# Kernel optimization log

Hardware: AMD Instinct MI355X
Metric: run time of the kernel (lower is better)

Reference implementation:

```python
import jax, jax.numpy as jnp
import numpy as np

T, B = 256, 256
OBS, FEAT, A = 512, 512, 15
H = FEAT + A + 1  # lstm_output_size = feature_dim + num_actions + 1 = 528


def setup_inputs() -> dict:
    key = jax.random.key(0)
    ks = jax.random.split(key, 16)
    s = 0.05
    f32 = jnp.float32
    return {
        "obs": jax.random.normal(ks[0], (T, B, OBS), f32),
        "last_action": jax.random.randint(ks[1], (T, B), 0, A, dtype=jnp.int32),
        "reward": jax.random.normal(ks[2], (T, B), f32),
        "terminated": jax.random.bernoulli(ks[3], 0.05, (T, B)),
        # encoder Linear(OBS -> FEAT)
        "W_enc": jax.random.normal(ks[4], (FEAT, OBS), f32) * s,
        "b_enc": jnp.zeros((FEAT,), f32),
        # 2-layer LSTM, input size == hidden size == H, torch gate order i,f,g,o
        "w_ih0": jax.random.normal(ks[5], (4 * H, H), f32) * s,
        "w_hh0": jax.random.normal(ks[6], (4 * H, H), f32) * s,
        "b_ih0": jnp.zeros((4 * H,), f32),
        "b_hh0": jnp.zeros((4 * H,), f32),
        "w_ih1": jax.random.normal(ks[7], (4 * H, H), f32) * s,
        "w_hh1": jax.random.normal(ks[8], (4 * H, H), f32) * s,
        "b_ih1": jnp.zeros((4 * H,), f32),
        "b_hh1": jnp.zeros((4 * H,), f32),
        # heads
        "W_pol": jax.random.normal(ks[9], (A, H), f32) * s,
        "b_pol": jnp.zeros((A,), f32),
        "W_base": jax.random.normal(ks[10], (1, H), f32) * s,
        "b_base": jnp.zeros((1,), f32),
    }


def reference(obs, last_action, reward, terminated,
              W_enc, b_enc,
              w_ih0, w_hh0, b_ih0, b_hh0,
              w_ih1, w_hh1, b_ih1, b_hh1,
              W_pol, b_pol, W_base, b_base):
    Tn, Bn = obs.shape[0], obs.shape[1]
    feats = jax.nn.relu(jnp.einsum('tbo,fo->tbf', obs, W_enc) + b_enc)
    one_hot = jax.nn.one_hot(last_action, A, dtype=feats.dtype)
    clipped_r = jnp.clip(reward, -1.0, 1.0)[..., None]
    x = jnp.concatenate([feats, clipped_r, one_hot], axis=-1)  # [T,B,H]
    nd = (~terminated).astype(x.dtype)[..., None]              # [T,B,1]

    w_ih = (w_ih0, w_ih1)
    w_hh = (w_hh0, w_hh1)
    b_ih = (b_ih0, b_ih1)
    b_hh = (b_hh0, b_hh1)

    def step(carry, inp):
        h, c = carry          # each [2,B,H]
        x_t, nd_t = inp       # [B,H], [B,1]
        h = h * nd_t          # done-mask reset of state, per original loop
        c = c * nd_t
        inp_l = x_t
        new_h, new_c = [], []
        for l in range(2):
            gates = inp_l @ w_ih[l].T + b_ih[l] + h[l] @ w_hh[l].T + b_hh[l]
            i, f, g, o = jnp.split(gates, 4, axis=-1)
            c_l = jax.nn.sigmoid(f) * c[l] + jax.nn.sigmoid(i) * jnp.tanh(g)
            h_l = jax.nn.sigmoid(o) * jnp.tanh(c_l)
            new_h.append(h_l)
            new_c.append(c_l)
            inp_l = h_l
        return (jnp.stack(new_h), jnp.stack(new_c)), inp_l

    h0 = jnp.zeros((2, Bn, H), x.dtype)  # init_state: zeros
    c0 = jnp.zeros((2, Bn, H), x.dtype)
    (hT, cT), lstm_out = jax.lax.scan(step, (h0, c0), (x, nd))  # lstm_out [T,B,H]

    policy_logits = lstm_out @ W_pol.T + b_pol          # [T,B,A]
    baseline = (lstm_out @ W_base.T + b_base)[..., 0]   # [T,B]
    action = jax.random.categorical(jax.random.key(1), policy_logits, axis=-1)  # [T,B]
    return policy_logits, baseline, action, hT, cT
```

## Files before the change

### kernel.cpp

```cpp
#include <hip/hip_runtime.h>
#include <stdint.h>
#include <math.h>

#define TSTEPS 256
#define BATCH  256
#define OBS_D  512
#define FEATD  512
#define NACT   15
#define HDIM   528
#define HB     (HDIM*BATCH)

#define OFF_ND    0
#define OFF_FLAG  65536
#define ALW_BYTES 262208
#define SB        91952
#define FXT       (SB)
#define FH0       (FXT + 4*HB)
#define FH1       (FH0 + 2*HB)
#define FC0       (FH1 + 2*HB)
#define FC1       (FC0 + HB)
#define FST_END   (FC1 + HB)

#define DBS0   0
#define DBS1   2112
#define DBENC  4224
#define DHW    4736
#define DHB    13184
#define DALW_N 13200

#define OUT_POL   0
#define OUT_BASE  983040
#define OUT_ACT   1048576
#define OUT_H     1114112
#define OUT_C     1384448

__device__ __forceinline__ float sigf_(float x){ return 1.0f/(1.0f+expf(-x)); }

__device__ __forceinline__ uint32_t rotl32_(uint32_t x, uint32_t d){
  return (x<<d)|(x>>(32u-d));
}

__device__ double gumbel_for(uint32_t idx){
  uint32_t x0 = 0u, x1 = idx;
  const uint32_t k0 = 0u, k1 = 1u;
  const uint32_t ks[3] = {k0, k1, 0x1BD11BDAu ^ k0 ^ k1};
  x0 += ks[0]; x1 += ks[1];
  const uint32_t R0[4] = {13u,15u,26u,6u}, R1[4] = {17u,29u,16u,24u};
  #pragma unroll
  for (int g=0; g<5; ++g){
    const uint32_t* r = (g&1) ? R1 : R0;
    #pragma unroll
    for (int j=0;j<4;++j){ x0 += x1; x1 = rotl32_(x1, r[j]); x1 ^= x0; }
    x0 += ks[(g+1)%3];
    x1 += ks[(g+2)%3] + (uint32_t)(g+1);
  }
  const uint32_t bits = x0 ^ x1;
  float u = __uint_as_float((bits>>9) | 0x3f800000u) - 1.0f;
  const float TINY = 1.17549435e-38f;
  u = u * (1.0f - TINY) + TINY;
  u = fmaxf(TINY, u);
  return -log(-log((double)u));
}

__global__ void zero_kernel(float* __restrict__ p, int n){
  int i = blockIdx.x*256 + threadIdx.x;
  if (i < n) p[i] = 0.0f;
}

__global__ void detect_term_kernel(const void* __restrict__ term, int* __restrict__ flag){
  __shared__ int s_nf, s_nb, s_ni;
  if (threadIdx.x==0){ s_nf=0; s_nb=0; s_ni=0; }
  __syncthreads();
  const uint8_t*  pb = (const uint8_t*)term;
  const uint32_t* pw = (const uint32_t*)term;
  int nf=0, nb=0, ni=0;
  for (int i=threadIdx.x; i<16384; i+=256){
    uint32_t v = pw[i];
    if (v == 0x3F800000u) nf++;
    if (v == 1u) ni++;
  }
  for (int o=threadIdx.x; o<65536; o+=256){
    if ((o&3) && pb[o]) nb++;
  }
  if (nf) atomicAdd(&s_nf, nf);
  if (nb) atomicAdd(&s_nb, nb);
  if (ni) atomicAdd(&s_ni, ni);
  __syncthreads();
  if (threadIdx.x==0){
    flag[0] = (s_nf>0) ? 2 : ((s_nb>0) ? 0 : ((s_ni>0) ? 1 : 0));
  }
}

__global__ void nd_kernel(const void* __restrict__ term, const int* __restrict__ flag,
                          float* __restrict__ nd){
  int i = blockIdx.x*256 + threadIdx.x;
  if (i >= TSTEPS*BATCH) return;
  int f = flag[0];
  bool done;
  if (f == 0)      done = ((const uint8_t*)term)[i] != 0;
  else if (f == 1) done = ((const int*)term)[i] != 0;
  else             done = ((const float*)term)[i] != 0.0f;
  nd[i] = done ? 0.0f : 1.0f;
}

__global__ void prep_small_kernel(float* __restrict__ alw,
    const float* __restrict__ bih0, const float* __restrict__ bhh0,
    const float* __restrict__ bih1, const float* __restrict__ bhh1,
    const float* __restrict__ benc,
    const float* __restrict__ Wpol, const float* __restrict__ bpol,
    const float* __restrict__ Wbase, const float* __restrict__ bbase){
  int i = blockIdx.x*256 + threadIdx.x;
  if (i >= DALW_N) return;
  if (i < 2112)            alw[DBS0 + i] = bih0[i] + bhh0[i];
  else if (i < 4224)       { int j=i-2112; alw[DBS1 + j] = bih1[j] + bhh1[j]; }
  else if (i < 4736)       { int j=i-4224; alw[DBENC + j] = benc[j]; }
  else if (i < 13184)      { int j=i-4736; int r=j/HDIM, k=j%HDIM;
                             alw[DHW + j] = (r<NACT ? Wpol[r*HDIM+k] : Wbase[k]); }
  else                     { int j=i-13184; alw[DHB + j] = (j<NACT ? bpol[j] : bbase[0]); }
}

__device__ __forceinline__ void lstm_block(
    int jt, int step, const float* __restrict__ srcA, const float* __restrict__ srcB,
    const float* __restrict__ wih, const float* __restrict__ whh,
    const float* __restrict__ bsum,
    const float* __restrict__ nd, float* __restrict__ cbuf, float* __restrict__ hout,
    int b)
{
  const int j0 = jt*2;
  const float ndv = nd[step*BATCH + b];
  float acc[8];
  const float* wA[8]; const float* wB[8];
  #pragma unroll
  for (int c=0;c<8;++c){
    const int col = (c>>1)*HDIM + j0 + (c&1);
    acc[c] = bsum[col];
    wA[c] = wih + (size_t)col*HDIM;
    wB[c] = whh + (size_t)col*HDIM;
  }
  const float* a = srcA + b;
  #pragma unroll 8
  for (int k=0;k<HDIM;++k){
    const float xv = a[(size_t)k*BATCH];
    #pragma unroll
    for (int c=0;c<8;++c) acc[c] = fmaf(wA[c][k], xv, acc[c]);
  }
  const float* bb = srcB + b;
  #pragma unroll 8
  for (int k=0;k<HDIM;++k){
    const float hv = bb[(size_t)k*BATCH] * ndv;
    #pragma unroll
    for (int c=0;c<8;++c) acc[c] = fmaf(wB[c][k], hv, acc[c]);
  }
  #pragma unroll
  for (int jj=0;jj<2;++jj){
    const float gi=acc[0+jj], gf=acc[2+jj], gg=acc[4+jj], go=acc[6+jj];
    const int idx=(j0+jj)*BATCH+b;
    const float cold = cbuf[idx]*ndv;
    const float cn = sigf_(gf)*cold + sigf_(gi)*tanhf(gg);
    const float hn = sigf_(go)*tanhf(cn);
    cbuf[idx]=cn; hout[idx]=hn;
  }
}

__global__ __launch_bounds__(256) void step_kernel(
  const float* __restrict__ obs, const int* __restrict__ lastAct,
  const float* __restrict__ reward,
  const float* __restrict__ wenc,
  const float* __restrict__ wih0, const float* __restrict__ whh0,
  const float* __restrict__ wih1, const float* __restrict__ whh1,
  float* __restrict__ ws, float* __restrict__ alw,
  float* __restrict__ out, int t)
{
  const int bid = blockIdx.x;
  const int b = threadIdx.x;
  float* nd = ws + OFF_ND;
  float* xT = ws + FXT;
  float* h0 = ws + FH0;
  float* h1 = ws + FH1;
  float* c0 = ws + FC0;
  float* c1 = ws + FC1;

  if (bid < 264) {
    if (t < 0 || t > 255) return;
    lstm_block(bid, t,
               xT + (size_t)(t&3)*HB,
               h0 + (size_t)((t+1)&1)*HB,
               wih0, whh0, alw + DBS0, nd, c0,
               h0 + (size_t)(t&1)*HB, b);
  } else if (bid < 528) {
    const int s = t - 1;
    if (s < 0 || s > 255) return;
    lstm_block(bid-264, s,
               h0 + (size_t)(s&1)*HB,
               h1 + (size_t)((s+1)&1)*HB,
               wih1, whh1, alw + DBS1, nd, c1,
               h1 + (size_t)(s&1)*HB, b);
  } else if (bid < 593) {
    const int te = t + 2;
    if (te < 0 || te > 255) return;
    float* xs = xT + (size_t)(te&3)*HB;
    if (bid < 592) {
      const int e = bid - 528;
      const int f0 = e*8;
      float acc[8];
      const float* wrow[8];
      #pragma unroll
      for (int c=0;c<8;++c){ acc[c]=alw[DBENC+f0+c]; wrow[c]=wenc+(size_t)(f0+c)*OBS_D; }
      __shared__ float lx[32][257];
      const int r0 = threadIdx.x>>3;
      const int kk = (threadIdx.x&7)<<2;
      for (int kc=0; kc<OBS_D; kc+=32){
        __syncthreads();
        #pragma unroll
        for (int rr=0; rr<256; rr+=32){
          const float4 v = *(const float4*)(obs + ((size_t)te*BATCH + (r0+rr))*OBS_D + kc + kk);
          lx[kk+0][r0+rr]=v.x; lx[kk+1][r0+rr]=v.y; lx[kk+2][r0+rr]=v.z; lx[kk+3][r0+rr]=v.w;
        }
        __syncthreads();
        #pragma unroll 4
        for (int k2=0;k2<32;++k2){
          const float xv = lx[k2][b];
          #pragma unroll
          for (int c=0;c<8;++c) acc[c] = fmaf(xv, wrow[c][kc+k2], acc[c]);
        }
      }
      #pragma unroll
      for (int c=0;c<8;++c) xs[(size_t)(f0+c)*BATCH + b] = fmaxf(acc[c], 0.0f);
    } else {
      const float r = reward[te*BATCH + b];
      xs[(size_t)FEATD*BATCH + b] = fminf(fmaxf(r, -1.0f), 1.0f);
      const int la = lastAct[te*BATCH + b];
      #pragma unroll
      for (int a2=0; a2<NACT; ++a2)
        xs[(size_t)(FEATD+1+a2)*BATCH + b] = (a2==la) ? 1.0f : 0.0f;
    }
  } else {
    const int s = t - 2;
    if (s < 0 || s > 255) return;
    const float* hsrc = h1 + (size_t)(s&1)*HB;
    float acc[16];
    #pragma unroll
    for (int c=0;c<16;++c) acc[c]=alw[DHB+c];
    const float* hb = hsrc + b;
    #pragma unroll 4
    for (int k=0;k<HDIM;++k){
      const float hv = hb[(size_t)k*BATCH];
      #pragma unroll
      for (int c=0;c<16;++c) acc[c] = fmaf(hv, alw[DHW + (size_t)c*HDIM + k], acc[c]);
    }
    const int row = s*BATCH + b;
    #pragma unroll
    for (int c=0;c<15;++c) out[OUT_POL + (size_t)row*NACT + c] = acc[c];
    out[OUT_BASE + row] = acc[15];
    double best = -1.0e300; int bi = 0;
    #pragma unroll
    for (int a2=0; a2<NACT; ++a2){
      const double v = (double)acc[a2] + gumbel_for((uint32_t)(row*NACT + a2));
      if (v > best){ best = v; bi = a2; }
    }
    out[OUT_ACT + row] = (float)bi;
  }
}

__global__ void finalize_kernel(const float* __restrict__ ws, float* __restrict__ out){
  int i = blockIdx.x*256 + threadIdx.x;
  if (i >= 2*HB) return;
  const int l = i / HB;
  const int r = i % HB;
  const int bq = r / HDIM;
  const int j  = r % HDIM;
  const float* hf = ws + (l==0 ? FH0 : FH1) + HB;
  const float* cf = ws + (l==0 ? FC0 : FC1);
  out[OUT_H + i] = hf[(size_t)j*BATCH + bq];
  out[OUT_C + i] = cf[(size_t)j*BATCH + bq];
}

extern "C" void kernel_launch(void* const* d_in, const int* in_sizes, int n_in,
                              void* d_out, int out_size, void* d_ws, size_t ws_size,
                              hipStream_t stream) {
  const float* obs     = (const float*)d_in[0];
  const int*   lastAct = (const int*)  d_in[1];
  const float* reward  = (const float*)d_in[2];
  const void*  term    =               d_in[3];
  const float* Wenc    = (const float*)d_in[4];
  const float* benc    = (const float*)d_in[5];
  const float* wih0    = (const float*)d_in[6];
  const float* whh0    = (const float*)d_in[7];
  const float* bih0    = (const float*)d_in[8];
  const float* bhh0    = (const float*)d_in[9];
  const float* wih1    = (const float*)d_in[10];
  const float* whh1    = (const float*)d_in[11];
  const float* bih1    = (const float*)d_in[12];
  const float* bhh1    = (const float*)d_in[13];
  const float* Wpol    = (const float*)d_in[14];
  const float* bpol    = (const float*)d_in[15];
  const float* Wbase   = (const float*)d_in[16];
  const float* bbase   = (const float*)d_in[17];
  float*  ws   = (float*)d_ws;
  int*    flag = (int*)(ws + OFF_FLAG);
  float*  alw  = (float*)((char*)d_ws + ALW_BYTES);
  float*  out  = (float*)d_out;

  {
    const int nz = 6*HB;
    zero_kernel<<<(nz+255)/256, 256, 0, stream>>>(ws + FH0, nz);
  }
  detect_term_kernel<<<1, 256, 0, stream>>>(term, flag);
  nd_kernel<<<(TSTEPS*BATCH+255)/256, 256, 0, stream>>>(term, flag, ws + OFF_ND);
  prep_small_kernel<<<(DALW_N+255)/256, 256, 0, stream>>>(alw,
      bih0, bhh0, bih1, bhh1, benc, Wpol, bpol, Wbase, bbase);

  for (int t = -2; t <= 257; ++t) {
    step_kernel<<<594, 256, 0, stream>>>(
      obs, lastAct, reward,
      Wenc, wih0, whh0, wih1, whh1,
      ws, alw, out, t);
  }
  finalize_kernel<<<(2*HB+255)/256, 256, 0, stream>>>(ws, out);
}
```

Before: 22.29 ms.

## Retile LSTM gate GEMV blocks with double-buffered shared-memory weight staging

Each LSTM block now covers 8 hidden units by 64 batch columns, not 2 hidden units by all 256 batch columns. Its weight rows are staged into shared memory in 128-wide K chunks, and the next chunk is prefetched into registers while the current one is consumed. Each thread computes 2 batch elements for one hidden unit across 4 gates with vectorized float4/float2 loads. This aims to cut redundant per-thread global weight reads and improve load coalescing. In exchange it adds barriers and shared-memory pressure, and the encoder now shares the same shared buffer.

```diff
diff --git a/kernel.cpp b/kernel.cpp
--- a/kernel.cpp
+++ b/kernel.cpp
@@ -9,6 +9,8 @@
 #define NACT   15
 #define HDIM   528
 #define HB     (HDIM*BATCH)
+#define JT     8
+#define BT     64
 
 #define OFF_ND    0
 #define OFF_FLAG  65536
@@ -19,7 +21,6 @@
 #define FH1       (FH0 + 2*HB)
 #define FC0       (FH1 + 2*HB)
 #define FC1       (FC0 + HB)
-#define FST_END   (FC1 + HB)
 
 #define DBS0   0
 #define DBS1   2112
@@ -119,46 +120,111 @@
   else                     { int j=i-13184; alw[DHB + j] = (j<NACT ? bpol[j] : bbase[0]); }
 }
 
-__device__ __forceinline__ void lstm_block(
-    int jt, int step, const float* __restrict__ srcA, const float* __restrict__ srcB,
+__device__ __forceinline__ void lstm32(
+    float* __restrict__ smem,
+    int tile, int bq, int step,
+    const float* __restrict__ srcA, const float* __restrict__ srcB,
     const float* __restrict__ wih, const float* __restrict__ whh,
-    const float* __restrict__ bsum,
-    const float* __restrict__ nd, float* __restrict__ cbuf, float* __restrict__ hout,
-    int b)
+    const float* __restrict__ bsum, const float* __restrict__ nd,
+    float* __restrict__ cbuf, float* __restrict__ hout)
 {
-  const int j0 = jt*2;
-  const float ndv = nd[step*BATCH + b];
-  float acc[8];
-  const float* wA[8]; const float* wB[8];
+  const int t = threadIdx.x;
+  const int p    = t & 31;
+  const int colg = t >> 5;
+  const int j0 = tile * JT;
+  const int b0 = bq * BT + 2*p;
+  const float nd0 = nd[step*BATCH + b0];
+  const float nd1 = nd[step*BATCH + b0 + 1];
+
+  const int rr  = t >> 3;
+  const int sg  = rr >> 3;
+  const int sj  = rr & 7;
+  const int kk0 = (t & 7) * 16;
+  const int kk0r= (t & 7) * 2;
+  const size_t srow = (size_t)(sg*HDIM + j0 + sj) * HDIM;
+
+  float acc[4][2];
   #pragma unroll
-  for (int c=0;c<8;++c){
-    const int col = (c>>1)*HDIM + j0 + (c&1);
-    acc[c] = bsum[col];
-    wA[c] = wih + (size_t)col*HDIM;
-    wB[c] = whh + (size_t)col*HDIM;
-  }
-  const float* a = srcA + b;
-  #pragma unroll 8
-  for (int k=0;k<HDIM;++k){
-    const float xv = a[(size_t)k*BATCH];
-    #pragma unroll
-    for (int c=0;c<8;++c) acc[c] = fmaf(wA[c][k], xv, acc[c]);
-  }
-  const float* bb = srcB + b;
-  #pragma unroll 8
-  for (int k=0;k<HDIM;++k){
-    const float hv = bb[(size_t)k*BATCH] * ndv;
-    #pragma unroll
-    for (int c=0;c<8;++c) acc[c] = fmaf(wB[c][k], hv, acc[c]);
-  }
+  for (int g=0; g<4; ++g){
+    const float bv = bsum[g*HDIM + j0 + colg];
+    acc[g][0] = bv; acc[g][1] = bv;
+  }
+
+  float4 s4[4]; float2 s2;
+
+  {
+    const float* wp = wih + srow;
+    #pragma unroll
+    for (int u=0; u<4; ++u) s4[u] = *(const float4*)(wp + kk0 + u*4);
+    #pragma unroll
+    for (int u=0; u<4; ++u) *(float4*)(smem + rr*132 + kk0 + u*4) = s4[u];
+  }
+  __syncthreads();
+
+  #pragma unroll 1
+  for (int cc=0; cc<10; ++cc){
+    const int pass = cc / 5;
+    const int ch   = cc % 5;
+    const int kc   = ch * 128;
+    const int klen = (ch==4) ? 16 : 128;
+    const int buf  = cc & 1;
+
+    const bool havenext = (cc+1) < 10;
+    if (havenext){
+      const int npass = (cc+1)/5, nch = (cc+1)%5;
+      const float* wp = (npass ? whh : wih) + srow + nch*128;
+      if (nch < 4){
+        #pragma unroll
+        for (int u=0; u<4; ++u) s4[u] = *(const float4*)(wp + kk0 + u*4);
+      } else {
+        s2 = *(const float2*)(wp + kk0r);
+      }
+    }
+
+    const float* asrc = (pass==0) ? srcA : srcB;
+    const float* lbase = smem + buf*4224;
+    #pragma unroll 2
+    for (int kk=0; kk<klen; kk+=4){
+      float4 wv[4];
+      #pragma unroll
+      for (int g=0; g<4; ++g)
+        wv[g] = *(const float4*)(lbase + (g*8+colg)*132 + kk);
+      const float* ap = asrc + (size_t)(kc+kk)*BATCH + b0;
+      #pragma unroll
+      for (int q=0; q<4; ++q){
+        float2 av = *(const float2*)(ap + (size_t)q*BATCH);
+        if (pass==1){ av.x *= nd0; av.y *= nd1; }
+        #pragma unroll
+        for (int g=0; g<4; ++g){
+          const float wq = ((const float*)&wv[g])[q];
+          acc[g][0] = fmaf(wq, av.x, acc[g][0]);
+          acc[g][1] = fmaf(wq, av.y, acc[g][1]);
+        }
+      }
+    }
+
+    if (havenext){
+      const int nbuf = (cc+1)&1, nch = (cc+1)%5;
+      float* wb = smem + nbuf*4224 + rr*132;
+      if (nch < 4){
+        #pragma unroll
+        for (int u=0; u<4; ++u) *(float4*)(wb + kk0 + u*4) = s4[u];
+      } else {
+        *(float2*)(wb + kk0r) = s2;
+      }
+    }
+    __syncthreads();
+  }
+
+  const int j = j0 + colg;
+  const int idx = j*BATCH + b0;
   #pragma unroll
-  for (int jj=0;jj<2;++jj){
-    const float gi=acc[0+jj], gf=acc[2+jj], gg=acc[4+jj], go=acc[6+jj];
-    const int idx=(j0+jj)*BATCH+b;
-    const float cold = cbuf[idx]*ndv;
-    const float cn = sigf_(gf)*cold + sigf_(gi)*tanhf(gg);
-    const float hn = sigf_(go)*tanhf(cn);
-    cbuf[idx]=cn; hout[idx]=hn;
+  for (int u=0; u<2; ++u){
+    const float ndv = u ? nd1 : nd0;
+    const float cold = cbuf[idx+u] * ndv;
+    const float cn = sigf_(acc[1][u])*cold + sigf_(acc[0][u])*tanhf(acc[2][u]);
+    const float hn = sigf_(acc[3][u])*tanhf(cn);
+    cbuf[idx+u] = cn; hout[idx+u] = hn;
   }
 }
 
@@ -171,6 +237,7 @@
   float* __restrict__ ws, float* __restrict__ alw,
   float* __restrict__ out, int t)
 {
+  __shared__ float smem[8448];
   const int bid = blockIdx.x;
   const int b = threadIdx.x;
   float* nd = ws + OFF_ND;
@@ -182,19 +249,20 @@
 
   if (bid < 264) {
     if (t < 0 || t > 255) return;
-    lstm_block(bid, t,
-               xT + (size_t)(t&3)*HB,
-               h0 + (size_t)((t+1)&1)*HB,
-               wih0, whh0, alw + DBS0, nd, c0,
-               h0 + (size_t)(t&1)*HB, b);
+    lstm32(smem, bid>>2, bid&3, t,
+           xT + (size_t)(t&3)*HB,
+           h0 + (size_t)((t+1)&1)*HB,
+           wih0, whh0, alw + DBS0, nd, c0,
+           h0 + (size_t)(t&1)*HB);
   } else if (bid < 528) {
     const int s = t - 1;
     if (s < 0 || s > 255) return;
-    lstm_block(bid-264, s,
-               h0 + (size_t)(s&1)*HB,
-               h1 + (size_t)((s+1)&1)*HB,
-               wih1, whh1, alw + DBS1, nd, c1,
-               h1 + (size_t)(s&1)*HB, b);
+    const int r = bid - 264;
+    lstm32(smem, r>>2, r&3, s,
+           h0 + (size_t)(s&1)*HB,
+           h1 + (size_t)((s+1)&1)*HB,
+           wih1, whh1, alw + DBS1, nd, c1,
+           h1 + (size_t)(s&1)*HB);
   } else if (bid < 593) {
     const int te = t + 2;
     if (te < 0 || te > 255) return;
@@ -206,7 +274,6 @@
       const float* wrow[8];
       #pragma unroll
       for (int c=0;c<8;++c){ acc[c]=alw[DBENC+f0+c]; wrow[c]=wenc+(size_t)(f0+c)*OBS_D; }
-      __shared__ float lx[32][257];
       const int r0 = threadIdx.x>>3;
       const int kk = (threadIdx.x&7)<<2;
       for (int kc=0; kc<OBS_D; kc+=32){
@@ -214,12 +281,13 @@
         #pragma unroll
         for (int rr=0; rr<256; rr+=32){
           const float4 v = *(const float4*)(obs + ((size_t)te*BATCH + (r0+rr))*OBS_D + kc + kk);
-          lx[kk+0][r0+rr]=v.x; lx[kk+1][r0+rr]=v.y; lx[kk+2][r0+rr]=v.z; lx[kk+3][r0+rr]=v.w;
+          smem[(kk+0)*257 + r0+rr]=v.x; smem[(kk+1)*257 + r0+rr]=v.y;
+          smem[(kk+2)*257 + r0+rr]=v.z; smem[(kk+3)*257 + r0+rr]=v.w;
         }
         __syncthreads();
         #pragma unroll 4
         for (int k2=0;k2<32;++k2){
-          const float xv = lx[k2][b];
+          const float xv = smem[k2*257 + b];
           #pragma unroll
           for (int c=0;c<8;++c) acc[c] = fmaf(xv, wrow[c][kc+k2], acc[c]);
         }
```

New measurement: 30.61 ms. 37.4% more time.

## Pack LSTM state buffers in 4-wide interleaved layout for float4 loads

Applied to the files above, without the earlier changes.

Changes the layout of the x, h and c workspace buffers from [k][batch] to [k/4][batch][4], so each thread reads four consecutive k values with a single float4 load. The LSTM gate loops, the head projection, the encoder output writes and finalize all switch to this packed indexing. The aim is fewer memory instructions per FMA. The trade-off is that each wavefront now touches a 4x wider span per load, and every reader and writer must agree on the new layout.

```diff
diff --git a/kernel.cpp b/kernel.cpp
--- a/kernel.cpp
+++ b/kernel.cpp
@@ -19,7 +19,6 @@
 #define FH1       (FH0 + 2*HB)
 #define FC0       (FH1 + 2*HB)
 #define FC1       (FC0 + HB)
-#define FST_END   (FC1 + HB)
 
 #define DBS0   0
 #define DBS1   2112
@@ -137,29 +136,51 @@
     wA[c] = wih + (size_t)col*HDIM;
     wB[c] = whh + (size_t)col*HDIM;
   }
-  const float* a = srcA + b;
-  #pragma unroll 8
-  for (int k=0;k<HDIM;++k){
-    const float xv = a[(size_t)k*BATCH];
-    #pragma unroll
-    for (int c=0;c<8;++c) acc[c] = fmaf(wA[c][k], xv, acc[c]);
-  }
-  const float* bb = srcB + b;
-  #pragma unroll 8
-  for (int k=0;k<HDIM;++k){
-    const float hv = bb[(size_t)k*BATCH] * ndv;
-    #pragma unroll
-    for (int c=0;c<8;++c) acc[c] = fmaf(wB[c][k], hv, acc[c]);
-  }
+
+  {
+    const float* ap = srcA + b*4;
+    #pragma unroll 2
+    for (int kq=0; kq<132; ++kq){
+      const float4 av = *(const float4*)(ap + (size_t)kq*(BATCH*4));
+      const int kb = kq*4;
+      const float xv[4] = {av.x, av.y, av.z, av.w};
+      #pragma unroll
+      for (int u=0;u<4;++u){
+        const float v = xv[u];
+        #pragma unroll
+        for (int c=0;c<8;++c) acc[c] = fmaf(wA[c][kb+u], v, acc[c]);
+      }
+    }
+  }
+
+  {
+    const float* hp = srcB + b*4;
+    #pragma unroll 2
+    for (int kq=0; kq<132; ++kq){
+      const float4 av = *(const float4*)(hp + (size_t)kq*(BATCH*4));
+      const int kb = kq*4;
+      const float xv[4] = {av.x, av.y, av.z, av.w};
+      #pragma unroll
+      for (int u=0;u<4;++u){
+        const float v = xv[u] * ndv;
+        #pragma unroll
+        for (int c=0;c<8;++c) acc[c] = fmaf(wB[c][kb+u], v, acc[c]);
+      }
+    }
+  }
+
+  const int base = (j0>>2)*(BATCH*4) + b*4 + (j0&3);
+  float cv[2], hv[2];
   #pragma unroll
   for (int jj=0;jj<2;++jj){
     const float gi=acc[0+jj], gf=acc[2+jj], gg=acc[4+jj], go=acc[6+jj];
-    const int idx=(j0+jj)*BATCH+b;
-    const float cold = cbuf[idx]*ndv;
+    const float cold = cbuf[base+jj]*ndv;
     const float cn = sigf_(gf)*cold + sigf_(gi)*tanhf(gg);
     const float hn = sigf_(go)*tanhf(cn);
-    cbuf[idx]=cn; hout[idx]=hn;
-  }
+    cv[jj]=cn; hv[jj]=hn;
+  }
+  *(float2*)(cbuf + base) = make_float2(cv[0], cv[1]);
+  *(float2*)(hout + base) = make_float2(hv[0], hv[1]);
 }
 
 __global__ __launch_bounds__(256) void step_kernel(
@@ -224,15 +245,24 @@
           for (int c=0;c<8;++c) acc[c] = fmaf(xv, wrow[c][kc+k2], acc[c]);
         }
       }
-      #pragma unroll
-      for (int c=0;c<8;++c) xs[(size_t)(f0+c)*BATCH + b] = fmaxf(acc[c], 0.0f);
+      const float4 o0 = make_float4(fmaxf(acc[0],0.0f), fmaxf(acc[1],0.0f),
+                                    fmaxf(acc[2],0.0f), fmaxf(acc[3],0.0f));
+      const float4 o1 = make_float4(fmaxf(acc[4],0.0f), fmaxf(acc[5],0.0f),
+                                    fmaxf(acc[6],0.0f), fmaxf(acc[7],0.0f));
+      *(float4*)(xs + (size_t)(f0>>2)*(BATCH*4) + b*4)     = o0;
+      *(float4*)(xs + (size_t)((f0>>2)+1)*(BATCH*4) + b*4) = o1;
     } else {
+      float vals[16];
       const float r = reward[te*BATCH + b];
-      xs[(size_t)FEATD*BATCH + b] = fminf(fmaxf(r, -1.0f), 1.0f);
+      vals[0] = fminf(fmaxf(r, -1.0f), 1.0f);
       const int la = lastAct[te*BATCH + b];
       #pragma unroll
-      for (int a2=0; a2<NACT; ++a2)
-        xs[(size_t)(FEATD+1+a2)*BATCH + b] = (a2==la) ? 1.0f : 0.0f;
+      for (int a2=0; a2<NACT; ++a2) vals[1+a2] = (a2==la) ? 1.0f : 0.0f;
+      #pragma unroll
+      for (int q=0; q<4; ++q){
+        const float4 o = make_float4(vals[q*4], vals[q*4+1], vals[q*4+2], vals[q*4+3]);
+        *(float4*)(xs + (size_t)(128+q)*(BATCH*4) + b*4) = o;
+      }
     }
   } else {
     const int s = t - 2;
@@ -241,12 +271,18 @@
     float acc[16];
     #pragma unroll
     for (int c=0;c<16;++c) acc[c]=alw[DHB+c];
-    const float* hb = hsrc + b;
-    #pragma unroll 4
-    for (int k=0;k<HDIM;++k){
-      const float hv = hb[(size_t)k*BATCH];
-      #pragma unroll
-      for (int c=0;c<16;++c) acc[c] = fmaf(hv, alw[DHW + (size_t)c*HDIM + k], acc[c]);
+    const float* hp = hsrc + b*4;
+    #pragma unroll 2
+    for (int kq=0; kq<132; ++kq){
+      const float4 hv4 = *(const float4*)(hp + (size_t)kq*(BATCH*4));
+      const int kb = kq*4;
+      const float hvv[4] = {hv4.x, hv4.y, hv4.z, hv4.w};
+      #pragma unroll
+      for (int u=0;u<4;++u){
+        const float hvu = hvv[u];
+        #pragma unroll
+        for (int c=0;c<16;++c) acc[c] = fmaf(hvu, alw[DHW + (size_t)c*HDIM + kb+u], acc[c]);
+      }
     }
     const int row = s*BATCH + b;
     #pragma unroll
@@ -271,8 +307,9 @@
   const int j  = r % HDIM;
   const float* hf = ws + (l==0 ? FH0 : FH1) + HB;
   const float* cf = ws + (l==0 ? FC0 : FC1);
-  out[OUT_H + i] = hf[(size_t)j*BATCH + bq];
-  out[OUT_C + i] = cf[(size_t)j*BATCH + bq];
+  const size_t pidx = (size_t)(j>>2)*(BATCH*4) + bq*4 + (j&3);
+  out[OUT_H + i] = hf[pidx];
+  out[OUT_C + i] = cf[pidx];
 }
 
 extern "C" void kernel_launch(void* const* d_in, const int* in_sizes, int n_in,
```

New measurement: 29.31 ms. +31.5%, slower.

## Register-tile LSTM gate GEMV over four batch columns per thread

Applied to the files above, without the earlier changes.

Each thread now computes the 8 gate accumulators for 4 consecutive batch entries, using float4 loads of inputs, hidden state, cell state and masks, so each weight load is reused four times. The LSTM blocks shrink from 264 to 66 per layer, with four 64-thread groups each handling a pair of hidden units, and the launch grid drops from 594 to 198 blocks. This cuts redundant weight loads and instruction count, at the cost of fewer blocks, which may underfill the GPU's compute units, and higher register pressure from 32 accumulators per thread.

```diff
diff --git a/kernel.cpp b/kernel.cpp
--- a/kernel.cpp
+++ b/kernel.cpp
@@ -19,7 +19,6 @@
 #define FH1       (FH0 + 2*HB)
 #define FC0       (FH1 + 2*HB)
 #define FC1       (FC0 + HB)
-#define FST_END   (FC1 + HB)
 
 #define DBS0   0
 #define DBS1   2112
@@ -119,46 +118,79 @@
   else                     { int j=i-13184; alw[DHB + j] = (j<NACT ? bpol[j] : bbase[0]); }
 }
 
-__device__ __forceinline__ void lstm_block(
-    int jt, int step, const float* __restrict__ srcA, const float* __restrict__ srcB,
+__device__ __forceinline__ void lstm_tile4(
+    int tile, int jl, int step,
+    const float* __restrict__ srcA, const float* __restrict__ srcB,
     const float* __restrict__ wih, const float* __restrict__ whh,
     const float* __restrict__ bsum,
     const float* __restrict__ nd, float* __restrict__ cbuf, float* __restrict__ hout,
-    int b)
+    int b0)
 {
-  const int j0 = jt*2;
-  const float ndv = nd[step*BATCH + b];
-  float acc[8];
+  const int j0 = tile*8 + jl*2;
+  float ndv[4];
+  {
+    const float4 n4 = *(const float4*)(nd + step*BATCH + b0);
+    ndv[0]=n4.x; ndv[1]=n4.y; ndv[2]=n4.z; ndv[3]=n4.w;
+  }
+  float acc[8][4];
   const float* wA[8]; const float* wB[8];
   #pragma unroll
   for (int c=0;c<8;++c){
     const int col = (c>>1)*HDIM + j0 + (c&1);
-    acc[c] = bsum[col];
+    const float bv = bsum[col];
+    #pragma unroll
+    for (int u=0;u<4;++u) acc[c][u] = bv;
     wA[c] = wih + (size_t)col*HDIM;
     wB[c] = whh + (size_t)col*HDIM;
   }
-  const float* a = srcA + b;
-  #pragma unroll 8
-  for (int k=0;k<HDIM;++k){
-    const float xv = a[(size_t)k*BATCH];
-    #pragma unroll
-    for (int c=0;c<8;++c) acc[c] = fmaf(wA[c][k], xv, acc[c]);
-  }
-  const float* bb = srcB + b;
-  #pragma unroll 8
-  for (int k=0;k<HDIM;++k){
-    const float hv = bb[(size_t)k*BATCH] * ndv;
-    #pragma unroll
-    for (int c=0;c<8;++c) acc[c] = fmaf(wB[c][k], hv, acc[c]);
-  }
+
+  {
+    const float* a = srcA + b0;
+    #pragma unroll 8
+    for (int k=0;k<HDIM;++k){
+      const float4 av = *(const float4*)(a + (size_t)k*BATCH);
+      const float xv[4] = {av.x, av.y, av.z, av.w};
+      #pragma unroll
+      for (int c=0;c<8;++c){
+        const float w = wA[c][k];
+        #pragma unroll
+        for (int u=0;u<4;++u) acc[c][u] = fmaf(w, xv[u], acc[c][u]);
+      }
+    }
+  }
+
+  {
+    const float* hbp = srcB + b0;
+    #pragma unroll 8
+    for (int k=0;k<HDIM;++k){
+      const float4 av = *(const float4*)(hbp + (size_t)k*BATCH);
+      float hv[4];
+      #pragma unroll
+      for (int u=0;u<4;++u) hv[u] = ((const float*)&av)[u] * ndv[u];
+      #pragma unroll
+      for (int c=0;c<8;++c){
+        const float w = wB[c][k];
+        #pragma unroll
+        for (int u=0;u<4;++u) acc[c][u] = fmaf(w, hv[u], acc[c][u]);
+      }
+    }
+  }
+
   #pragma unroll
   for (int jj=0;jj<2;++jj){
-    const float gi=acc[0+jj], gf=acc[2+jj], gg=acc[4+jj], go=acc[6+jj];
-    const int idx=(j0+jj)*BATCH+b;
-    const float cold = cbuf[idx]*ndv;
-    const float cn = sigf_(gf)*cold + sigf_(gi)*tanhf(gg);
-    const float hn = sigf_(go)*tanhf(cn);
-    cbuf[idx]=cn; hout[idx]=hn;
+    const int idx = (j0+jj)*BATCH + b0;
+    const float4 co = *(const float4*)(cbuf + idx);
+    float cv[4], hv2[4];
+    #pragma unroll
+    for (int u=0;u<4;++u){
+      const float gi=acc[0+jj][u], gf=acc[2+jj][u], gg=acc[4+jj][u], go=acc[6+jj][u];
+      const float cold = ((const float*)&co)[u]*ndv[u];
+      const float cn = sigf_(gf)*cold + sigf_(gi)*tanhf(gg);
+      const float hn = sigf_(go)*tanhf(cn);
+      cv[u]=cn; hv2[u]=hn;
+    }
+    *(float4*)(cbuf + idx) = make_float4(cv[0],cv[1],cv[2],cv[3]);
+    *(float4*)(hout + idx) = make_float4(hv2[0],hv2[1],hv2[2],hv2[3]);
   }
 }
 
@@ -180,27 +212,27 @@
   float* c0 = ws + FC0;
   float* c1 = ws + FC1;
 
-  if (bid < 264) {
+  if (bid < 66) {
     if (t < 0 || t > 255) return;
-    lstm_block(bid, t,
+    lstm_tile4(bid, b>>6, t,
                xT + (size_t)(t&3)*HB,
                h0 + (size_t)((t+1)&1)*HB,
                wih0, whh0, alw + DBS0, nd, c0,
-               h0 + (size_t)(t&1)*HB, b);
-  } else if (bid < 528) {
+               h0 + (size_t)(t&1)*HB, (b&63)*4);
+  } else if (bid < 132) {
     const int s = t - 1;
     if (s < 0 || s > 255) return;
-    lstm_block(bid-264, s,
+    lstm_tile4(bid-66, b>>6, s,
                h0 + (size_t)(s&1)*HB,
                h1 + (size_t)((s+1)&1)*HB,
                wih1, whh1, alw + DBS1, nd, c1,
-               h1 + (size_t)(s&1)*HB, b);
-  } else if (bid < 593) {
+               h1 + (size_t)(s&1)*HB, (b&63)*4);
+  } else if (bid < 197) {
     const int te = t + 2;
     if (te < 0 || te > 255) return;
     float* xs = xT + (size_t)(te&3)*HB;
-    if (bid < 592) {
-      const int e = bid - 528;
+    if (bid < 196) {
+      const int e = bid - 132;
       const int f0 = e*8;
       float acc[8];
       const float* wrow[8];
@@ -311,7 +343,7 @@
       bih0, bhh0, bih1, bhh1, benc, Wpol, bpol, Wbase, bbase);
 
   for (int t = -2; t <= 257; ++t) {
-    step_kernel<<<594, 256, 0, stream>>>(
+    step_kernel<<<198, 256, 0, stream>>>(
       obs, lastAct, reward,
       Wenc, wih0, whh0, wih1, whh1,
       ws, alw, out, t);
```

Result: slower. 37.60 ms (+68.7%).
